# Optimization experiments

Measured on AMD Instinct MI355X. Metric: run time of the kernel, lower is better.

## Reference

```python
import jax, jax.numpy as jnp
import numpy as np

B, C, L = 32, 64, 2048
FREQ = L // 2 + 1            # 1025
BAND_SIZES = [341, 341, 343]  # freq//3, freq//3, remainder


def setup_inputs() -> dict:
    key = jax.random.key(0)
    k = jax.random.split(key, 6)
    X = jax.random.normal(k[0], (B, C, L), dtype=jnp.float32)
    A0 = jax.random.normal(k[1], (BAND_SIZES[0], BAND_SIZES[0]), dtype=jnp.float32)
    A1 = jax.random.normal(k[2], (BAND_SIZES[1], BAND_SIZES[1]), dtype=jnp.float32)
    A2 = jax.random.normal(k[3], (BAND_SIZES[2], BAND_SIZES[2]), dtype=jnp.float32)
    fusion_weights = jnp.ones((3,), dtype=jnp.float32)
    # Gumbel(0,1) noise for the 2-way gumbel-softmax over each (b, i, j) entry
    gumbel_noise = jax.random.gumbel(k[4], (B, C, C, 2), dtype=jnp.float32)
    return {"X": X, "A0": A0, "A1": A1, "A2": A2,
            "fusion_weights": fusion_weights, "gumbel_noise": gumbel_noise}


def _band_dist(band, A):
    # band: (b, c, s), A: (s, s). dist[b,i,j] = ||A (band_i - band_j)||^2
    # Gram trick: ||y_i - y_j||^2 = q_i + q_j - 2 y_i . y_j, y = band @ A^T
    Y = jnp.einsum('ds,bcs->bcd', A, band)          # (b, c, s)
    G = jnp.einsum('bid,bjd->bij', Y, Y)            # (b, c, c)
    q = jnp.einsum('bid,bid->bi', Y, Y)             # (b, c)
    dist = q[:, :, None] + q[:, None, :] - 2.0 * G
    return jnp.maximum(dist, 0.0)                   # guard fp round-off


def reference(X, A0, A1, A2, fusion_weights, gumbel_noise):
    XF = jnp.abs(jnp.fft.rfft(X, axis=-1))          # (b, c, FREQ)
    s0, s1, s2 = BAND_SIZES
    bands = (XF[..., :s0], XF[..., s0:s0 + s1], XF[..., s0 + s1:])
    As = (A0, A1, A2)
    dists = jnp.stack([_band_dist(b_, A_) for b_, A_ in zip(bands, As)], axis=-1)  # (b,c,c,3)
    w = jax.nn.softmax(fusion_weights)
    dist = jnp.einsum('bijk,k->bij', dists, w)      # (b, c, c)

    exp_dist = 1.0 / (dist + 1e-10)
    eye = jnp.eye(C, dtype=exp_dist.dtype)
    mask = 1.0 - eye
    exp_dist = exp_dist * mask
    exp_max = jax.lax.stop_gradient(jnp.max(exp_dist, axis=-1, keepdims=True))
    p = exp_dist / exp_max
    p = (p * mask + eye) * 0.99                     # probs in (0, 0.99]

    # Bernoulli via 2-class gumbel-softmax (hard, tau=1, straight-through)
    logits = jnp.stack([jnp.log(p / (1.0 - p)), jnp.log((1.0 - p) / p)], axis=-1)  # (b,c,c,2)
    y = logits + gumbel_noise
    y_soft = jax.nn.softmax(y, axis=-1)
    y_hard = jax.nn.one_hot(jnp.argmax(y, axis=-1), 2, dtype=y_soft.dtype)
    sample = (y_hard - jax.lax.stop_gradient(y_soft) + y_soft)[..., 0]  # (b,c,c)
    return sample[:, None, :, :]                    # (b, 1, c, c)
```

## Files before the change

### kernel.cpp

```cpp
#include <hip/hip_runtime.h>
#include <math.h>

#define Bn 32
#define Cn 64
#define Ln 2048
#define NFREQ 1025
#define S0c 341
#define S1c 341
#define S2c 343

#define PI_D 3.14159265358979323846

typedef double v4d __attribute__((ext_vector_type(4)));

#define PADIX(i) ((i) + ((i) >> 4))

__global__ void k_twiddle(double2* __restrict__ tw) {
    int t = blockIdx.x * blockDim.x + threadIdx.x;
    if (t < 2048) {
        double ang = -2.0 * PI_D * (double)t / 2048.0;
        double s, c;
        sincos(ang, &s, &c);
        tw[t] = make_double2(c, s);
    }
}

__device__ __forceinline__ int rev4_10(unsigned x) {
    unsigned t = __brev(x) >> 22;
    return (int)(((t & 0x155u) << 1) | ((t >> 1) & 0x155u));
}

__global__ __launch_bounds__(256) void k_fft(const float* __restrict__ X,
                                             const double2* __restrict__ tw,
                                             float* __restrict__ XF) {
    __shared__ double re[1088];
    __shared__ double im[1088];
    int row = blockIdx.x;
    int tid = threadIdx.x;
    {
        int k = tid;
        double2 w1 = tw[2 * k];
        double2 w2 = tw[4 * k];
        double2 w3 = tw[6 * k];
        int i0 = PADIX(k), i1 = PADIX(k + 256), i2 = PADIX(k + 512), i3 = PADIX(k + 768);
        const float2* xr = (const float2*)(X + (size_t)row * Ln);
        float2 v0 = xr[k];
        float2 v1 = xr[k + 256];
        float2 v2 = xr[k + 512];
        float2 v3 = xr[k + 768];
        double ar = (double)v0.x, ai = (double)v0.y;
        double br = (double)v1.x, bi = (double)v1.y;
        double cr = (double)v2.x, ci = (double)v2.y;
        double dr = (double)v3.x, di = (double)v3.y;
        double t0r = ar + cr, t0i = ai + ci;
        double t1r = ar - cr, t1i = ai - ci;
        double t2r = br + dr, t2i = bi + di;
        double t3r = br - dr, t3i = bi - di;
        re[i0] = t0r + t2r; im[i0] = t0i + t2i;
        double u1r = t1r + t3i, u1i = t1i - t3r;
        re[i1] = u1r * w1.x - u1i * w1.y; im[i1] = u1r * w1.y + u1i * w1.x;
        double u2r = t0r - t2r, u2i = t0i - t2i;
        re[i2] = u2r * w2.x - u2i * w2.y; im[i2] = u2r * w2.y + u2i * w2.x;
        double u3r = t1r - t3i, u3i = t1i + t3r;
        re[i3] = u3r * w3.x - u3i * w3.y; im[i3] = u3r * w3.y + u3i * w3.x;
    }
    __syncthreads();
    #pragma unroll
    for (int s = 1; s < 5; ++s) {
        int log2Q = 8 - 2 * s;
        int Q = 1 << log2Q;
        int k = tid & (Q - 1);
        int g = tid >> log2Q;
        int base = (g << (log2Q + 2)) + k;
        int i0 = PADIX(base), i1 = PADIX(base + Q), i2 = PADIX(base + 2 * Q), i3 = PADIX(base + 3 * Q);
        int step = 2 << (2 * s);
        double2 w1 = tw[k * step];
        double2 w2 = tw[2 * k * step];
        double2 w3 = tw[3 * k * step];
        double ar = re[i0], ai = im[i0];
        double br = re[i1], bi = im[i1];
        double cr = re[i2], ci = im[i2];
        double dr = re[i3], di = im[i3];
        double t0r = ar + cr, t0i = ai + ci;
        double t1r = ar - cr, t1i = ai - ci;
        double t2r = br + dr, t2i = bi + di;
        double t3r = br - dr, t3i = bi - di;
        re[i0] = t0r + t2r; im[i0] = t0i + t2i;
        double u1r = t1r + t3i, u1i = t1i - t3r;
        re[i1] = u1r * w1.x - u1i * w1.y; im[i1] = u1r * w1.y + u1i * w1.x;
        double u2r = t0r - t2r, u2i = t0i - t2i;
        re[i2] = u2r * w2.x - u2i * w2.y; im[i2] = u2r * w2.y + u2i * w2.x;
        double u3r = t1r - t3i, u3i = t1i + t3r;
        re[i3] = u3r * w3.x - u3i * w3.y; im[i3] = u3r * w3.y + u3i * w3.x;
        __syncthreads();
    }
    float* out0 = XF + (size_t)row * NFREQ;
    for (int k = tid; k <= 1024; k += 256) {
        double Xr, Xi;
        if (k == 0)        { Xr = re[0] + im[0]; Xi = 0.0; }
        else if (k == 1024){ Xr = re[0] - im[0]; Xi = 0.0; }
        else {
            int rv  = PADIX(rev4_10((unsigned)k));
            int rv2 = PADIX(rev4_10((unsigned)(1024 - k)));
            double2 t = tw[k];
            double Zr = re[rv],  Zi = im[rv];
            double Wr = re[rv2], Wi = im[rv2];
            double Er = 0.5 * (Zr + Wr), Ei = 0.5 * (Zi - Wi);
            double Or = 0.5 * (Zi + Wi), Oi = -0.5 * (Zr - Wr);
            Xr = Er + t.x * Or - t.y * Oi;
            Xi = Ei + t.x * Oi + t.y * Or;
        }
        out0[k] = (float)sqrt(Xr * Xr + Xi * Xi);
    }
}

__global__ __launch_bounds__(256) void k_gemm(const float* __restrict__ XF,
                                              const float* __restrict__ A0,
                                              const float* __restrict__ A1,
                                              const float* __restrict__ A2,
                                              double* __restrict__ Y) {
    const int Sarr[3] = {S0c, S1c, S2c};
    const int Oarr[3] = {0, S0c, S0c + S1c};
    int bz = blockIdx.z;
    int z = bz >> 2, q = bz & 3;
    const float* A = (z == 0) ? A0 : ((z == 1) ? A1 : A2);
    int S = Sarr[z], O = Oarr[z];
    int qm = q >> 1, qn = q & 1;

    __shared__ float sX[32][34];
    __shared__ float sA[32][34];
    int r0 = blockIdx.x * 64 + qm * 32;
    int d0 = blockIdx.y * 64 + qn * 32;
    int tid = threadIdx.x;
    int lane = tid & 63, w = tid >> 6;
    int lm = (w >> 1) * 16, ln = (w & 1) * 16;
    int fm = lane & 15, kq = lane >> 4;
    int kl = tid & 31, rl = tid >> 5;

    v4d zero = {0.0, 0.0, 0.0, 0.0};
    double aval = (double)fm;
    v4d calR = __builtin_amdgcn_mfma_f64_16x16x4f64(aval, 1.0, zero, 0, 0, 0);
    v4d calC = __builtin_amdgcn_mfma_f64_16x16x4f64(1.0, aval, zero, 0, 0, 0);
    int rIdx[4], cIdx[4];
    #pragma unroll
    for (int i = 0; i < 4; ++i) {
        rIdx[i] = (int)(calR[i] * 0.25);
        cIdx[i] = (int)(calC[i] * 0.25);
    }

    auto load_tile = [&](int st, float* px, float* pa) {
        int ss = st * 32 + kl;
        bool sv = ss < S;
        #pragma unroll
        for (int i = 0; i < 4; ++i)
            px[i] = sv ? XF[(size_t)(r0 + rl + 8 * i) * NFREQ + O + ss] : 0.0f;
        #pragma unroll
        for (int j = 0; j < 4; ++j) {
            int d = d0 + rl + 8 * j;
            pa[j] = (sv && d < S) ? A[(size_t)d * S + ss] : 0.0f;
        }
    };

    v4d acc = zero;
    float px[4], pa[4];
    load_tile(0, px, pa);
    int nsteps = (S + 31) / 32;
    for (int st = 0; st < nsteps; ++st) {
        __syncthreads();
        #pragma unroll
        for (int i = 0; i < 4; ++i) sX[rl + 8 * i][kl] = px[i];
        #pragma unroll
        for (int j = 0; j < 4; ++j) sA[rl + 8 * j][kl] = pa[j];
        __syncthreads();
        if (st + 1 < nsteps) load_tile(st + 1, px, pa);
        #pragma unroll
        for (int t = 0; t < 8; ++t) {
            int k = 4 * t + kq;
            double a = (double)sX[lm + fm][k];
            double b = (double)sA[ln + fm][k];
            acc = __builtin_amdgcn_mfma_f64_16x16x4f64(a, b, acc, 0, 0, 0);
        }
    }
    #pragma unroll
    for (int i = 0; i < 4; ++i) {
        int row = r0 + lm + rIdx[i];
        int d = d0 + ln + cIdx[i];
        if (d < S) Y[(size_t)row * NFREQ + O + d] = acc[i];
    }
}

__global__ __launch_bounds__(256) void k_dist(const double* __restrict__ Y,
                                              const float* __restrict__ fw,
                                              double* __restrict__ part) {
    __shared__ double sY[64][34];
    int b = blockIdx.x;
    int chunk = blockIdx.y;
    int dlo = chunk * 128;
    int dhi = (chunk == 7) ? NFREQ : dlo + 128;
    int tid = threadIdx.x;
    int lane = tid & 63, w = tid >> 6;
    int wm = (w >> 1) * 32, wn = (w & 1) * 32;
    int fm = lane & 15, kq = lane >> 4;
    int kl = tid & 31, rl = tid >> 5;

    double f0 = (double)fw[0], f1 = (double)fw[1], f2 = (double)fw[2];
    double m = fmax(f0, fmax(f1, f2));
    double e0 = exp(f0 - m), e1 = exp(f1 - m), e2 = exp(f2 - m);
    double esum = e0 + e1 + e2;
    double sw0 = sqrt(e0 / esum), sw1 = sqrt(e1 / esum), sw2 = sqrt(e2 / esum);

    v4d zero = {0.0, 0.0, 0.0, 0.0};
    double aval = (double)fm;
    v4d calR = __builtin_amdgcn_mfma_f64_16x16x4f64(aval, 1.0, zero, 0, 0, 0);
    v4d calC = __builtin_amdgcn_mfma_f64_16x16x4f64(1.0, aval, zero, 0, 0, 0);
    int rIdx[4], cIdx[4];
    #pragma unroll
    for (int i = 0; i < 4; ++i) {
        rIdx[i] = (int)(calR[i] * 0.25);
        cIdx[i] = (int)(calC[i] * 0.25);
    }

    const double* Yb = Y + (size_t)b * Cn * NFREQ;
    auto load_tile = [&](int k0, double* py) {
        int d = dlo + k0 + kl;
        bool dv = d < dhi;
        double sw = dv ? ((d < S0c) ? sw0 : ((d < S0c + S1c) ? sw1 : sw2)) : 0.0;
        #pragma unroll
        for (int i = 0; i < 8; ++i)
            py[i] = dv ? Yb[(size_t)(rl + 8 * i) * NFREQ + d] * sw : 0.0;
    };

    v4d acc00 = zero, acc01 = zero, acc10 = zero, acc11 = zero;
    double py[8];
    load_tile(0, py);
    int nsteps = (dhi - dlo + 31) / 32;
    for (int st = 0; st < nsteps; ++st) {
        __syncthreads();
        #pragma unroll
        for (int i = 0; i < 8; ++i) sY[rl + 8 * i][kl] = py[i];
        __syncthreads();
        if (st + 1 < nsteps) load_tile((st + 1) * 32, py);
        #pragma unroll
        for (int t = 0; t < 8; ++t) {
            int k = 4 * t + kq;
            double a0 = sY[wm + fm][k];
            double a1 = sY[wm + 16 + fm][k];
            double b0 = sY[wn + fm][k];
            double b1 = sY[wn + 16 + fm][k];
            acc00 = __builtin_amdgcn_mfma_f64_16x16x4f64(a0, b0, acc00, 0, 0, 0);
            acc01 = __builtin_amdgcn_mfma_f64_16x16x4f64(a0, b1, acc01, 0, 0, 0);
            acc10 = __builtin_amdgcn_mfma_f64_16x16x4f64(a1, b0, acc10, 0, 0, 0);
            acc11 = __builtin_amdgcn_mfma_f64_16x16x4f64(a1, b1, acc11, 0, 0, 0);
        }
    }
    double* pb = part + (((size_t)b * 8 + chunk) << 12);
    #pragma unroll
    for (int i = 0; i < 4; ++i) {
        int rowA = wm + rIdx[i], rowB = rowA + 16;
        int cA = wn + cIdx[i], cB = cA + 16;
        pb[rowA * 64 + cA] = acc00[i];
        pb[rowA * 64 + cB] = acc01[i];
        pb[rowB * 64 + cA] = acc10[i];
        pb[rowB * 64 + cB] = acc11[i];
    }
}

__global__ __launch_bounds__(256) void k_decide(const double* __restrict__ part,
                                                const float* __restrict__ gum,
                                                float* __restrict__ out) {
    __shared__ double sQ[64];
    int b = blockIdx.x;
    int tid = threadIdx.x;
    const double* pb = part + (((size_t)b * 8) << 12);
    if (tid < 64) {
        double q = 0.0;
        #pragma unroll
        for (int c = 0; c < 8; ++c) q += pb[((size_t)c << 12) + tid * 65];
        sQ[tid] = q;
    }
    __syncthreads();
    int i = blockIdx.y * 4 + (tid >> 6);
    int j = tid & 63;
    double g = 0.0;
    #pragma unroll
    for (int c = 0; c < 8; ++c) g += pb[((size_t)c << 12) + i * 64 + j];
    double dist = fmax(sQ[i] + sQ[j] - 2.0 * g, 0.0);
    double e = (i == j) ? 0.0 : 1.0 / (dist + 1e-10);
    double emax = e;
    #pragma unroll
    for (int off = 32; off; off >>= 1)
        emax = fmax(emax, __shfl_xor(emax, off, 64));
    double p = (i == j) ? 0.99 : (e / emax) * 0.99;
    double l0 = log(p / (1.0 - p));
    double l1 = log((1.0 - p) / p);
    int idx = i * 64 + j;
    const float* gb = gum + (size_t)b * 8192;
    double y0 = l0 + (double)gb[2 * idx];
    double y1 = l1 + (double)gb[2 * idx + 1];
    out[(size_t)b * 4096 + idx] = (y0 >= y1) ? 1.0f : 0.0f;
}

extern "C" void kernel_launch(void* const* d_in, const int* in_sizes, int n_in,
                              void* d_out, int out_size, void* d_ws, size_t ws_size,
                              hipStream_t stream) {
    const float* X  = (const float*)d_in[0];
    const float* A0 = (const float*)d_in[1];
    const float* A1 = (const float*)d_in[2];
    const float* A2 = (const float*)d_in[3];
    const float* fw = (const float*)d_in[4];
    const float* gm = (const float*)d_in[5];
    float* out = (float*)d_out;

    char* ws = (char*)d_ws;
    double2* tw  = (double2*)(ws);
    float*   XF  = (float*)(ws + 32768);
    double*  Y   = (double*)(ws + 8429568);
    double*  part = (double*)(ws + 32768);

    k_twiddle<<<8, 256, 0, stream>>>(tw);
    k_fft<<<Bn * Cn, 256, 0, stream>>>(X, tw, XF);
    k_gemm<<<dim3(32, 6, 12), 256, 0, stream>>>(XF, A0, A1, A2, Y);
    k_dist<<<dim3(Bn, 8), 256, 0, stream>>>(Y, fw, part);
    k_decide<<<dim3(Bn, 16), 256, 0, stream>>>(part, gm, out);
}
```

Before: 161.1 us.

## Replace FP64 MFMA projection GEMM with split-bf16 triple-product MFMAs

The band projection GEMM stops using f64 16x16x4 MFMAs. Each fp32 input is split into three bf16 parts, and six bf16 16x16x32 MFMA products per K-tile approximate fp32 precision, with per-tile partial sums accumulated in double. Shared-memory tiles become bf16 with vectorised stores and loads. The aim is to use the much higher bf16 matrix throughput instead of the slow fp64 path, at the cost of extra split arithmetic, more LDS traffic and a small precision change that could flip near-threshold Bernoulli outputs. The second logit is also computed as the negation of the first instead of a second log.

```diff
diff --git a/kernel.cpp b/kernel.cpp
--- a/kernel.cpp
+++ b/kernel.cpp
@@ -12,8 +12,28 @@
 #define PI_D 3.14159265358979323846
 
 typedef double v4d __attribute__((ext_vector_type(4)));
+typedef unsigned short u16;
+typedef __attribute__((ext_vector_type(4))) u16 u16x4;
+typedef __attribute__((ext_vector_type(8))) short short8;
+typedef __attribute__((ext_vector_type(4))) float f32x4;
 
 #define PADIX(i) ((i) + ((i) >> 4))
+
+__device__ __forceinline__ u16 rneb(float f) {
+    unsigned u = __float_as_uint(f);
+    unsigned r = (u + 0x7FFFu + ((u >> 16) & 1u)) >> 16;
+    return (u16)r;
+}
+__device__ __forceinline__ float b2f(u16 h) {
+    return __uint_as_float(((unsigned)h) << 16);
+}
+__device__ __forceinline__ void split3(float v, u16& h1, u16& h2, u16& h3) {
+    h1 = rneb(v);
+    float r1 = v - b2f(h1);
+    h2 = rneb(r1);
+    float r2 = r1 - b2f(h2);
+    h3 = rneb(r2);
+}
 
 __global__ void k_twiddle(double2* __restrict__ tw) {
     int t = blockIdx.x * blockDim.x + threadIdx.x;
@@ -127,65 +147,87 @@
     int S = Sarr[z], O = Oarr[z];
     int qm = q >> 1, qn = q & 1;
 
-    __shared__ float sX[32][34];
-    __shared__ float sA[32][34];
+    __shared__ u16 sX1[32][40], sX2[32][40], sX3[32][40];
+    __shared__ u16 sA1[32][40], sA2[32][40], sA3[32][40];
+
     int r0 = blockIdx.x * 64 + qm * 32;
     int d0 = blockIdx.y * 64 + qn * 32;
     int tid = threadIdx.x;
     int lane = tid & 63, w = tid >> 6;
     int lm = (w >> 1) * 16, ln = (w & 1) * 16;
     int fm = lane & 15, kq = lane >> 4;
-    int kl = tid & 31, rl = tid >> 5;
-
-    v4d zero = {0.0, 0.0, 0.0, 0.0};
-    double aval = (double)fm;
-    v4d calR = __builtin_amdgcn_mfma_f64_16x16x4f64(aval, 1.0, zero, 0, 0, 0);
-    v4d calC = __builtin_amdgcn_mfma_f64_16x16x4f64(1.0, aval, zero, 0, 0, 0);
+    int row8 = tid >> 3, seg4 = (tid & 7) * 4;
+
+    f32x4 z4 = {0.0f, 0.0f, 0.0f, 0.0f};
+    short8 aone, afm;
+    {
+        u16 hone = 0x3F80;
+        u16 hfm = rneb((float)fm);
+        #pragma unroll
+        for (int j = 0; j < 8; ++j) { aone[j] = (short)hone; afm[j] = (short)hfm; }
+    }
+    f32x4 calR = __builtin_amdgcn_mfma_f32_16x16x32_bf16(afm, aone, z4, 0, 0, 0);
+    f32x4 calC = __builtin_amdgcn_mfma_f32_16x16x32_bf16(aone, afm, z4, 0, 0, 0);
     int rIdx[4], cIdx[4];
     #pragma unroll
     for (int i = 0; i < 4; ++i) {
-        rIdx[i] = (int)(calR[i] * 0.25);
-        cIdx[i] = (int)(calC[i] * 0.25);
-    }
-
-    auto load_tile = [&](int st, float* px, float* pa) {
-        int ss = st * 32 + kl;
-        bool sv = ss < S;
-        #pragma unroll
-        for (int i = 0; i < 4; ++i)
-            px[i] = sv ? XF[(size_t)(r0 + rl + 8 * i) * NFREQ + O + ss] : 0.0f;
+        rIdx[i] = (int)(calR[i] * 0.03125f + 0.5f);
+        cIdx[i] = (int)(calC[i] * 0.03125f + 0.5f);
+    }
+
+    u16x4 wx1, wx2, wx3, wa1, wa2, wa3;
+    auto load_tile = [&](int st) {
+        int ss0 = st * 32 + seg4;
+        const float* xrow = XF + (size_t)(r0 + row8) * NFREQ + O;
+        int dA = d0 + row8;
+        bool dv = dA < S;
+        const float* arow = A + (size_t)dA * S;
         #pragma unroll
         for (int j = 0; j < 4; ++j) {
-            int d = d0 + rl + 8 * j;
-            pa[j] = (sv && d < S) ? A[(size_t)d * S + ss] : 0.0f;
+            int ss = ss0 + j;
+            bool sv = ss < S;
+            float xv = sv ? xrow[ss] : 0.0f;
+            float av = (sv && dv) ? arow[ss] : 0.0f;
+            u16 h1, h2, h3;
+            split3(xv, h1, h2, h3); wx1[j] = h1; wx2[j] = h2; wx3[j] = h3;
+            split3(av, h1, h2, h3); wa1[j] = h1; wa2[j] = h2; wa3[j] = h3;
         }
     };
 
-    v4d acc = zero;
-    float px[4], pa[4];
-    load_tile(0, px, pa);
+    double accd[4] = {0.0, 0.0, 0.0, 0.0};
+    load_tile(0);
     int nsteps = (S + 31) / 32;
     for (int st = 0; st < nsteps; ++st) {
         __syncthreads();
-        #pragma unroll
-        for (int i = 0; i < 4; ++i) sX[rl + 8 * i][kl] = px[i];
-        #pragma unroll
-        for (int j = 0; j < 4; ++j) sA[rl + 8 * j][kl] = pa[j];
-        __syncthreads();
-        if (st + 1 < nsteps) load_tile(st + 1, px, pa);
-        #pragma unroll
-        for (int t = 0; t < 8; ++t) {
-            int k = 4 * t + kq;
-            double a = (double)sX[lm + fm][k];
-            double b = (double)sA[ln + fm][k];
-            acc = __builtin_amdgcn_mfma_f64_16x16x4f64(a, b, acc, 0, 0, 0);
-        }
+        *(u16x4*)&sX1[row8][seg4] = wx1;
+        *(u16x4*)&sX2[row8][seg4] = wx2;
+        *(u16x4*)&sX3[row8][seg4] = wx3;
+        *(u16x4*)&sA1[row8][seg4] = wa1;
+        *(u16x4*)&sA2[row8][seg4] = wa2;
+        *(u16x4*)&sA3[row8][seg4] = wa3;
+        __syncthreads();
+        if (st + 1 < nsteps) load_tile(st + 1);
+        short8 a1 = *(const short8*)&sX1[lm + fm][kq * 8];
+        short8 a2 = *(const short8*)&sX2[lm + fm][kq * 8];
+        short8 a3 = *(const short8*)&sX3[lm + fm][kq * 8];
+        short8 b1 = *(const short8*)&sA1[ln + fm][kq * 8];
+        short8 b2 = *(const short8*)&sA2[ln + fm][kq * 8];
+        short8 b3 = *(const short8*)&sA3[ln + fm][kq * 8];
+        f32x4 p1 = __builtin_amdgcn_mfma_f32_16x16x32_bf16(a1, b1, z4, 0, 0, 0);
+        f32x4 p2 = __builtin_amdgcn_mfma_f32_16x16x32_bf16(a1, b2, z4, 0, 0, 0);
+        p2 = __builtin_amdgcn_mfma_f32_16x16x32_bf16(a2, b1, p2, 0, 0, 0);
+        p2 = __builtin_amdgcn_mfma_f32_16x16x32_bf16(a1, b3, p2, 0, 0, 0);
+        p2 = __builtin_amdgcn_mfma_f32_16x16x32_bf16(a2, b2, p2, 0, 0, 0);
+        p2 = __builtin_amdgcn_mfma_f32_16x16x32_bf16(a3, b1, p2, 0, 0, 0);
+        #pragma unroll
+        for (int i = 0; i < 4; ++i)
+            accd[i] += (double)p1[i] + (double)p2[i];
     }
     #pragma unroll
     for (int i = 0; i < 4; ++i) {
         int row = r0 + lm + rIdx[i];
         int d = d0 + ln + cIdx[i];
-        if (d < S) Y[(size_t)row * NFREQ + O + d] = acc[i];
+        if (d < S) Y[(size_t)row * NFREQ + O + d] = accd[i];
     }
 }
 
@@ -292,7 +334,7 @@
         emax = fmax(emax, __shfl_xor(emax, off, 64));
     double p = (i == j) ? 0.99 : (e / emax) * 0.99;
     double l0 = log(p / (1.0 - p));
-    double l1 = log((1.0 - p) / p);
+    double l1 = -l0;
     int idx = i * 64 + j;
     const float* gb = gum + (size_t)b * 8192;
     double y0 = l0 + (double)gb[2 * idx];
```

New measurement: 160.3 us. About the same (-0.4%).
